# Optimization experiments

Hardware: AMD Instinct MI355X
Metric: run time of the kernel (lower is better)

The kernel has to match this reference:

```python
import jax, jax.numpy as jnp
import numpy as np

B, IN, OUT = 4, 32, 64
N, NS = 163842, 40962  # icosahedron mesh levels: NS = (N + 6) / 4
EPS = 1e-5
SLOPE = 0.2


def setup_inputs() -> dict:
    key = jax.random.key(0)
    ks = jax.random.split(key, 8)
    x = jax.random.normal(ks[0], (B, IN, N), dtype=jnp.float32)
    x1 = jax.random.normal(ks[1], (B, OUT, NS), dtype=jnp.float32)
    pool_neigh = jax.random.randint(ks[2], (NS * 7,), 0, N, dtype=jnp.int32)
    neigh = jax.random.randint(ks[3], (NS * 7,), 0, NS, dtype=jnp.int32)
    W1 = jax.random.normal(ks[4], (OUT, 7 * IN), dtype=jnp.float32) / np.sqrt(7 * IN).astype(np.float32)
    b1 = jnp.zeros((OUT,), dtype=jnp.float32)
    gamma = jnp.ones((OUT,), dtype=jnp.float32)
    beta = jnp.zeros((OUT,), dtype=jnp.float32)
    Wc = jax.random.normal(ks[5], (OUT, 2 * OUT), dtype=jnp.float32) / np.sqrt(2 * OUT).astype(np.float32)
    bc = jnp.zeros((OUT,), dtype=jnp.float32)
    return dict(x=x, x1=x1, pool_neigh=pool_neigh, neigh=neigh,
                W1=W1, b1=b1, gamma=gamma, beta=beta, Wc=Wc, bc=bc)


def reference(x, x1, pool_neigh, neigh, W1, b1, gamma, beta, Wc, bc):
    b, c, n = x.shape
    ns = (n + 6) // 4
    # pool_layer_batch ('mean'): gather 7-neighborhood on fine mesh, mean-pool
    pooled = x[:, :, pool_neigh[: ns * 7]].reshape(b, c, ns, 7).mean(axis=3)  # [B, IN, NS]
    # onering_conv_layer_batch: gather 7-stencil, reshape to [B, NS, 7*IN], linear
    mat = pooled[:, :, neigh].reshape(b, c, ns, 7)          # [B, IN, NS, 7]
    mat = mat.transpose(0, 2, 3, 1).reshape(b, ns, 7 * c)   # [B, NS, 7*IN]
    h = jnp.einsum('bnk,ok->bon', mat, W1) + b1[None, :, None]  # [B, OUT, NS]
    # BatchNorm1d (track_running_stats=False -> always batch stats) + LeakyReLU(0.2)
    mu = h.mean(axis=(0, 2), keepdims=True)
    var = h.var(axis=(0, 2), keepdims=True)
    h = gamma[None, :, None] * (h - mu) * jax.lax.rsqrt(var + EPS) + beta[None, :, None]
    h = jnp.where(h >= 0, h, SLOPE * h)
    # concat skip + 1x1 Conv1d
    cat = jnp.concatenate([h, x1], axis=1)                  # [B, 2*OUT, NS]
    out = jnp.einsum('bcn,oc->bon', cat, Wc) + bc[None, :, None]
    return out
```

## Files before the change

kernel.cpp:

```cpp
#include <hip/hip_runtime.h>
#include <cstddef>

#define NB    4
#define CIN   32
#define COUT  64
#define NFINE 163842
#define NSV   40962
#define EPSB  1e-5f
#define SLOPE 0.2f

typedef __attribute__((ext_vector_type(8))) short short8;
typedef __attribute__((ext_vector_type(4))) float f32x4;

#define O_XT   ((size_t)0)
#define O_H    ((size_t)0)
#define O_POOL ((size_t)48 << 20)
#define O_W1F  ((size_t)60 << 20)
#define O_WCF  ((size_t)60 << 20 | 0x8000)
#define O_ST   ((size_t)61 << 20)

static __device__ __forceinline__ short f2bf(float f) {
    union { float f; unsigned u; } v; v.f = f;
    unsigned r = v.u + 0x7fffu + ((v.u >> 16) & 1u);
    return (short)(r >> 16);
}
static __device__ __forceinline__ float bf2f(short h) {
    union { unsigned u; float f; } v;
    v.u = ((unsigned)(unsigned short)h) << 16;
    return v.f;
}

__global__ void k_prep(const float* __restrict__ W1, const float* __restrict__ Wc,
                       short* __restrict__ W1f, short* __restrict__ Wcf,
                       float* __restrict__ stats) {
    if (threadIdx.x < 128) stats[threadIdx.x] = 0.f;
    for (int i = threadIdx.x; i < 7 * 4 * 64 * 8; i += 256) {
        int e = i & 7, l = (i >> 3) & 63, nf = (i >> 9) & 3, kk = i >> 11;
        int o = 16 * nf + (l & 15);
        int k = 32 * kk + 8 * (l >> 4) + e;
        W1f[i] = f2bf(W1[o * (7 * CIN) + k]);
    }
    for (int i = threadIdx.x; i < 4 * 4 * 64 * 8; i += 256) {
        int e = i & 7, l = (i >> 3) & 63, nf = (i >> 9) & 3, kk = i >> 11;
        int o = 16 * nf + (l & 15);
        int c = 32 * kk + 8 * (l >> 4) + e;
        Wcf[i] = f2bf(Wc[o * (2 * COUT) + c]);
    }
}

__global__ __launch_bounds__(256) void k_transpose(
        const float* __restrict__ x, short* __restrict__ xt) {
    __shared__ float tile[128][33];
    const int n0 = blockIdx.x * 128;
    const int b  = blockIdx.y;
    const float* xb = x + (size_t)b * CIN * NFINE;
#pragma unroll
    for (int q = 0; q < 16; ++q) {
        int i = threadIdx.x + 256 * q;
        int c = i >> 7, nl = i & 127;
        int n = n0 + nl;
        tile[nl][c] = (n < NFINE) ? xb[(size_t)c * NFINE + n] : 0.f;
    }
    __syncthreads();
#pragma unroll
    for (int q = 0; q < 2; ++q) {
        int i = threadIdx.x + 256 * q;
        int nl = i >> 2, cg = i & 3;
        int n = n0 + nl;
        if (n >= NFINE) continue;
        short8 o;
#pragma unroll
        for (int e = 0; e < 8; ++e) o[e] = f2bf(tile[nl][8 * cg + e]);
        *(short8*)(xt + ((size_t)b * NFINE + n) * CIN + 8 * cg) = o;
    }
}

__global__ __launch_bounds__(256) void k_pool(
        const short* __restrict__ xt, const int* __restrict__ pn,
        short* __restrict__ pooled) {
    const int s = blockIdx.x * 256 + threadIdx.x;
    const int b = blockIdx.y;
    if (s >= NSV) return;
    int t[7];
#pragma unroll
    for (int j = 0; j < 7; ++j) t[j] = pn[7 * s + j];
    const short* xb = xt + (size_t)b * NFINE * CIN;
    short* op = pooled + ((size_t)b * NSV + s) * CIN;
#pragma unroll
    for (int gq = 0; gq < 4; ++gq) {
        short8 v[7];
#pragma unroll
        for (int j = 0; j < 7; ++j)
            v[j] = *(const short8*)(xb + (size_t)t[j] * CIN + 8 * gq);
        float a8[8];
#pragma unroll
        for (int e = 0; e < 8; ++e) a8[e] = 0.f;
#pragma unroll
        for (int j = 0; j < 7; ++j)
#pragma unroll
            for (int e = 0; e < 8; ++e) a8[e] += bf2f(v[j][e]);
        short8 o;
#pragma unroll
        for (int e = 0; e < 8; ++e) o[e] = f2bf(a8[e] * (1.f / 7.f));
        *(short8*)(op + 8 * gq) = o;
    }
}

__global__ __launch_bounds__(256) void k_conv(
        const int* __restrict__ neigh, const short* __restrict__ W1f,
        const short* __restrict__ pooled, short* __restrict__ hbf,
        float* __restrict__ stats) {
    __shared__ float red[2][4][COUT];
    const int l = threadIdx.x & 63, w = threadIdx.x >> 6;
    const int b = blockIdx.y;
    const int s0 = blockIdx.x * 128 + w * 32;
    const int r = l & 15, g = l >> 4;

    const short* pb = pooled + (size_t)b * NSV * CIN;
    const int sA0 = s0 + r, sA1 = s0 + 16 + r;
    const bool v0 = sA0 < NSV, v1 = sA1 < NSV;
    const int c0 = v0 ? sA0 : NSV - 1, c1 = v1 ? sA1 : NSV - 1;

    int t0[7], t1[7];
#pragma unroll
    for (int kk = 0; kk < 7; ++kk) { t0[kk] = neigh[7 * c0 + kk]; t1[kk] = neigh[7 * c1 + kk]; }

    short8 a0[7], a1[7];
#pragma unroll
    for (int kk = 0; kk < 7; ++kk) {
        a0[kk] = *(const short8*)(pb + (size_t)t0[kk] * CIN + 8 * g);
        a1[kk] = *(const short8*)(pb + (size_t)t1[kk] * CIN + 8 * g);
    }

    f32x4 acc[2][4];
#pragma unroll
    for (int mf = 0; mf < 2; ++mf)
#pragma unroll
        for (int nf = 0; nf < 4; ++nf) acc[mf][nf] = (f32x4){0.f, 0.f, 0.f, 0.f};

#pragma unroll
    for (int kk = 0; kk < 7; ++kk) {
        const short8* wf = (const short8*)(W1f) + (size_t)kk * 256;
#pragma unroll
        for (int nf = 0; nf < 4; ++nf) {
            short8 bfv = wf[nf * 64 + l];
            acc[0][nf] = __builtin_amdgcn_mfma_f32_16x16x32_bf16(a0[kk], bfv, acc[0][nf], 0, 0, 0);
            acc[1][nf] = __builtin_amdgcn_mfma_f32_16x16x32_bf16(a1[kk], bfv, acc[1][nf], 0, 0, 0);
        }
    }

    float sum[4], sq[4];
#pragma unroll
    for (int nf = 0; nf < 4; ++nf) { sum[nf] = 0.f; sq[nf] = 0.f; }
#pragma unroll
    for (int mf = 0; mf < 2; ++mf)
#pragma unroll
        for (int nf = 0; nf < 4; ++nf) {
            f32x4 d = acc[mf][nf];
#pragma unroll
            for (int rr = 0; rr < 4; ++rr) {
                const int srow = s0 + 16 * mf + 4 * g + rr;
                const float v = d[rr];
                const bool ok = srow < NSV;
                if (ok) hbf[((size_t)b * NSV + srow) * COUT + 16 * nf + r] = f2bf(v);
                const float vm = ok ? v : 0.f;
                sum[nf] += vm; sq[nf] += vm * vm;
            }
        }
#pragma unroll
    for (int nf = 0; nf < 4; ++nf) {
        float a = sum[nf], c = sq[nf];
        a += __shfl_xor(a, 16); a += __shfl_xor(a, 32);
        c += __shfl_xor(c, 16); c += __shfl_xor(c, 32);
        if (g == 0) { red[0][w][16 * nf + r] = a; red[1][w][16 * nf + r] = c; }
    }
    __syncthreads();
    if (threadIdx.x < COUT) {
        const int o = threadIdx.x;
        atomicAdd(&stats[o],        red[0][0][o] + red[0][1][o] + red[0][2][o] + red[0][3][o]);
        atomicAdd(&stats[COUT + o], red[1][0][o] + red[1][1][o] + red[1][2][o] + red[1][3][o]);
    }
}

__global__ void k_stats(const float* __restrict__ gamma,
                        const float* __restrict__ beta, float* __restrict__ st) {
    const int o = threadIdx.x;
    const float cnt = (float)((size_t)NB * NSV);
    float mu  = st[o] / cnt;
    float var = st[COUT + o] / cnt - mu * mu;
    float sc  = gamma[o] * rsqrtf(var + EPSB);
    st[2 * COUT + o] = sc;
    st[3 * COUT + o] = beta[o] - mu * sc;
}

__global__ __launch_bounds__(256) void k_out(
        const short* __restrict__ hbf, const float* __restrict__ x1,
        const short* __restrict__ Wcf, const float* __restrict__ st,
        const float* __restrict__ bc, float* __restrict__ out) {
    __shared__ __attribute__((aligned(16))) short Wcs[4 * 4 * 64 * 8];
    __shared__ float scs[COUT], shs[COUT], bcs[COUT];
    {
        const short8* src = (const short8*)Wcf;
        short8* dst = (short8*)Wcs;
        for (int i = threadIdx.x; i < 1024; i += 256) dst[i] = src[i];
        if (threadIdx.x < COUT) {
            scs[threadIdx.x] = st[2 * COUT + threadIdx.x];
            shs[threadIdx.x] = st[3 * COUT + threadIdx.x];
            bcs[threadIdx.x] = bc[threadIdx.x];
        }
    }
    __syncthreads();

    const int l = threadIdx.x & 63, w = threadIdx.x >> 6;
    const int b = blockIdx.y;
    const int s0 = blockIdx.x * 128 + w * 32;
    const int r = l & 15, g = l >> 4;

    int sa0 = s0 + r;       if (sa0 > NSV - 1) sa0 = NSV - 1;
    int sa1 = s0 + 16 + r;  if (sa1 > NSV - 1) sa1 = NSV - 1;
    const size_t rowA0 = ((size_t)b * NSV + sa0) * COUT;
    const size_t rowA1 = ((size_t)b * NSV + sa1) * COUT;

    short8 h00 = *(const short8*)(hbf + rowA0 + 8 * g);
    short8 h01 = *(const short8*)(hbf + rowA0 + 32 + 8 * g);
    short8 h10 = *(const short8*)(hbf + rowA1 + 8 * g);
    short8 h11 = *(const short8*)(hbf + rowA1 + 32 + 8 * g);
    const float* x1b = x1 + (size_t)b * COUT * NSV;
    float xv0[16], xv1[16];
#pragma unroll
    for (int i = 0; i < 16; ++i) {
        const int c2 = 32 * (i >> 3) + 8 * g + (i & 7);
        xv0[i] = x1b[(size_t)c2 * NSV + sa0];
        xv1[i] = x1b[(size_t)c2 * NSV + sa1];
    }

    float scv[16], shv[16];
#pragma unroll
    for (int kk = 0; kk < 2; ++kk)
#pragma unroll
        for (int e = 0; e < 8; ++e) {
            scv[8 * kk + e] = scs[32 * kk + 8 * g + e];
            shv[8 * kk + e] = shs[32 * kk + 8 * g + e];
        }

    f32x4 acc[2][4];
#pragma unroll
    for (int mf = 0; mf < 2; ++mf)
#pragma unroll
        for (int nf = 0; nf < 4; ++nf) acc[mf][nf] = (f32x4){0.f, 0.f, 0.f, 0.f};

#pragma unroll
    for (int kk = 0; kk < 4; ++kk) {
        short8 a0, a1;
        if (kk < 2) {
            short8 hh0 = kk ? h01 : h00;
            short8 hh1 = kk ? h11 : h10;
#pragma unroll
            for (int e = 0; e < 8; ++e) {
                float z0 = scv[8 * kk + e] * bf2f(hh0[e]) + shv[8 * kk + e];
                float z1 = scv[8 * kk + e] * bf2f(hh1[e]) + shv[8 * kk + e];
                z0 = fmaxf(z0, SLOPE * z0);
                z1 = fmaxf(z1, SLOPE * z1);
                a0[e] = f2bf(z0); a1[e] = f2bf(z1);
            }
        } else {
#pragma unroll
            for (int e = 0; e < 8; ++e) {
                a0[e] = f2bf(xv0[8 * (kk - 2) + e]);
                a1[e] = f2bf(xv1[8 * (kk - 2) + e]);
            }
        }
        const short8* wf = (const short8*)Wcs + kk * 4 * 64;
#pragma unroll
        for (int nf = 0; nf < 4; ++nf) {
            short8 bfv = wf[nf * 64 + l];
            acc[0][nf] = __builtin_amdgcn_mfma_f32_16x16x32_bf16(a0, bfv, acc[0][nf], 0, 0, 0);
            acc[1][nf] = __builtin_amdgcn_mfma_f32_16x16x32_bf16(a1, bfv, acc[1][nf], 0, 0, 0);
        }
    }

    float* ob = out + (size_t)b * COUT * NSV;
#pragma unroll
    for (int mf = 0; mf < 2; ++mf)
#pragma unroll
        for (int nf = 0; nf < 4; ++nf) {
            const int o  = 16 * nf + r;
            const int sr = s0 + 16 * mf + 4 * g;
            f32x4 d = acc[mf][nf];
            const float bb = bcs[o];
            float* p = ob + (size_t)o * NSV + sr;
            if (sr + 3 < NSV) {
                *(float2*)(p)     = make_float2(d[0] + bb, d[1] + bb);
                *(float2*)(p + 2) = make_float2(d[2] + bb, d[3] + bb);
            } else {
#pragma unroll
                for (int rr = 0; rr < 4; ++rr)
                    if (sr + rr < NSV) p[rr] = d[rr] + bb;
            }
        }
}

extern "C" void kernel_launch(void* const* d_in, const int* in_sizes, int n_in,
                              void* d_out, int out_size, void* d_ws, size_t ws_size,
                              hipStream_t stream) {
    const float* x          = (const float*)d_in[0];
    const float* x1         = (const float*)d_in[1];
    const int*   pool_neigh = (const int*)d_in[2];
    const int*   neigh      = (const int*)d_in[3];
    const float* W1         = (const float*)d_in[4];
    const float* gamma      = (const float*)d_in[6];
    const float* beta       = (const float*)d_in[7];
    const float* Wc         = (const float*)d_in[8];
    const float* bc         = (const float*)d_in[9];

    char* wsb = (char*)d_ws;
    short* xt     = (short*)(wsb + O_XT);
    short* hbf    = (short*)(wsb + O_H);
    short* pooled = (short*)(wsb + O_POOL);
    short* W1f    = (short*)(wsb + O_W1F);
    short* Wcf    = (short*)(wsb + O_WCF);
    float* stats  = (float*)(wsb + O_ST);
    float* out    = (float*)d_out;

    k_prep<<<1, 256, 0, stream>>>(W1, Wc, W1f, Wcf, stats);
    k_transpose<<<dim3((NFINE + 127) / 128, NB), 256, 0, stream>>>(x, xt);
    k_pool<<<dim3((NSV + 255) / 256, NB), 256, 0, stream>>>(xt, pool_neigh, pooled);
    k_conv<<<dim3((NSV + 127) / 128, NB), 256, 0, stream>>>(neigh, W1f, pooled, hbf, stats);
    k_stats<<<1, 64, 0, stream>>>(gamma, beta, stats);
    k_out<<<dim3((NSV + 127) / 128, NB), 256, 0, stream>>>(hbf, x1, Wcf, stats, bc, out);
}
```

Measured before the change: 342.9 us.

## Fold prep and stats kernels into neighbors; split pool work per channel group

Weight repacking and stats zeroing move into block (0,0) of the transpose kernel, and the BN scale/shift finalization moves into each k_out block's prologue. Together these remove two small kernel launches. The pool kernel now gives each thread one 8-channel group instead of all four, so there are four times as many threads and more gathers in flight. The cost is one transpose block doing extra serial work, every k_out block recomputing the stats, and each pool thread reloading its 7 neighbor indices.

```diff
diff --git a/kernel.cpp b/kernel.cpp
--- a/kernel.cpp
+++ b/kernel.cpp
@@ -30,26 +30,11 @@
     return v.f;
 }
 
-__global__ void k_prep(const float* __restrict__ W1, const float* __restrict__ Wc,
-                       short* __restrict__ W1f, short* __restrict__ Wcf,
-                       float* __restrict__ stats) {
-    if (threadIdx.x < 128) stats[threadIdx.x] = 0.f;
-    for (int i = threadIdx.x; i < 7 * 4 * 64 * 8; i += 256) {
-        int e = i & 7, l = (i >> 3) & 63, nf = (i >> 9) & 3, kk = i >> 11;
-        int o = 16 * nf + (l & 15);
-        int k = 32 * kk + 8 * (l >> 4) + e;
-        W1f[i] = f2bf(W1[o * (7 * CIN) + k]);
-    }
-    for (int i = threadIdx.x; i < 4 * 4 * 64 * 8; i += 256) {
-        int e = i & 7, l = (i >> 3) & 63, nf = (i >> 9) & 3, kk = i >> 11;
-        int o = 16 * nf + (l & 15);
-        int c = 32 * kk + 8 * (l >> 4) + e;
-        Wcf[i] = f2bf(Wc[o * (2 * COUT) + c]);
-    }
-}
-
 __global__ __launch_bounds__(256) void k_transpose(
-        const float* __restrict__ x, short* __restrict__ xt) {
+        const float* __restrict__ x, short* __restrict__ xt,
+        const float* __restrict__ W1, const float* __restrict__ Wc,
+        short* __restrict__ W1f, short* __restrict__ Wcf,
+        float* __restrict__ stats) {
     __shared__ float tile[128][33];
     const int n0 = blockIdx.x * 128;
     const int b  = blockIdx.y;
@@ -73,37 +58,49 @@
         for (int e = 0; e < 8; ++e) o[e] = f2bf(tile[nl][8 * cg + e]);
         *(short8*)(xt + ((size_t)b * NFINE + n) * CIN + 8 * cg) = o;
     }
+    if (blockIdx.x == 0 && blockIdx.y == 0) {
+        if (threadIdx.x < 128) stats[threadIdx.x] = 0.f;
+        for (int i = threadIdx.x; i < 7 * 4 * 64 * 8; i += 256) {
+            int e = i & 7, l = (i >> 3) & 63, nf = (i >> 9) & 3, kk = i >> 11;
+            int o = 16 * nf + (l & 15);
+            int k = 32 * kk + 8 * (l >> 4) + e;
+            W1f[i] = f2bf(W1[o * (7 * CIN) + k]);
+        }
+        for (int i = threadIdx.x; i < 4 * 4 * 64 * 8; i += 256) {
+            int e = i & 7, l = (i >> 3) & 63, nf = (i >> 9) & 3, kk = i >> 11;
+            int o = 16 * nf + (l & 15);
+            int c = 32 * kk + 8 * (l >> 4) + e;
+            Wcf[i] = f2bf(Wc[o * (2 * COUT) + c]);
+        }
+    }
 }
 
 __global__ __launch_bounds__(256) void k_pool(
         const short* __restrict__ xt, const int* __restrict__ pn,
         short* __restrict__ pooled) {
-    const int s = blockIdx.x * 256 + threadIdx.x;
+    const int gid = blockIdx.x * 256 + threadIdx.x;
+    const int s = gid >> 2, gq = gid & 3;
     const int b = blockIdx.y;
     if (s >= NSV) return;
     int t[7];
 #pragma unroll
     for (int j = 0; j < 7; ++j) t[j] = pn[7 * s + j];
-    const short* xb = xt + (size_t)b * NFINE * CIN;
-    short* op = pooled + ((size_t)b * NSV + s) * CIN;
-#pragma unroll
-    for (int gq = 0; gq < 4; ++gq) {
-        short8 v[7];
-#pragma unroll
-        for (int j = 0; j < 7; ++j)
-            v[j] = *(const short8*)(xb + (size_t)t[j] * CIN + 8 * gq);
-        float a8[8];
-#pragma unroll
-        for (int e = 0; e < 8; ++e) a8[e] = 0.f;
-#pragma unroll
-        for (int j = 0; j < 7; ++j)
-#pragma unroll
-            for (int e = 0; e < 8; ++e) a8[e] += bf2f(v[j][e]);
-        short8 o;
-#pragma unroll
-        for (int e = 0; e < 8; ++e) o[e] = f2bf(a8[e] * (1.f / 7.f));
-        *(short8*)(op + 8 * gq) = o;
-    }
+    const short* xb = xt + (size_t)b * NFINE * CIN + 8 * gq;
+    short8 v[7];
+#pragma unroll
+    for (int j = 0; j < 7; ++j)
+        v[j] = *(const short8*)(xb + (size_t)t[j] * CIN);
+    float a8[8];
+#pragma unroll
+    for (int e = 0; e < 8; ++e) a8[e] = 0.f;
+#pragma unroll
+    for (int j = 0; j < 7; ++j)
+#pragma unroll
+        for (int e = 0; e < 8; ++e) a8[e] += bf2f(v[j][e]);
+    short8 o;
+#pragma unroll
+    for (int e = 0; e < 8; ++e) o[e] = f2bf(a8[e] * (1.f / 7.f));
+    *(short8*)(pooled + ((size_t)b * NSV + s) * CIN + 8 * gq) = o;
 }
 
 __global__ __launch_bounds__(256) void k_conv(
@@ -182,20 +179,10 @@
     }
 }
 
-__global__ void k_stats(const float* __restrict__ gamma,
-                        const float* __restrict__ beta, float* __restrict__ st) {
-    const int o = threadIdx.x;
-    const float cnt = (float)((size_t)NB * NSV);
-    float mu  = st[o] / cnt;
-    float var = st[COUT + o] / cnt - mu * mu;
-    float sc  = gamma[o] * rsqrtf(var + EPSB);
-    st[2 * COUT + o] = sc;
-    st[3 * COUT + o] = beta[o] - mu * sc;
-}
-
 __global__ __launch_bounds__(256) void k_out(
         const short* __restrict__ hbf, const float* __restrict__ x1,
         const short* __restrict__ Wcf, const float* __restrict__ st,
+        const float* __restrict__ gamma, const float* __restrict__ beta,
         const float* __restrict__ bc, float* __restrict__ out) {
     __shared__ __attribute__((aligned(16))) short Wcs[4 * 4 * 64 * 8];
     __shared__ float scs[COUT], shs[COUT], bcs[COUT];
@@ -204,9 +191,14 @@
         short8* dst = (short8*)Wcs;
         for (int i = threadIdx.x; i < 1024; i += 256) dst[i] = src[i];
         if (threadIdx.x < COUT) {
-            scs[threadIdx.x] = st[2 * COUT + threadIdx.x];
-            shs[threadIdx.x] = st[3 * COUT + threadIdx.x];
-            bcs[threadIdx.x] = bc[threadIdx.x];
+            const int o = threadIdx.x;
+            const float cnt = (float)((size_t)NB * NSV);
+            float mu  = st[o] / cnt;
+            float var = st[COUT + o] / cnt - mu * mu;
+            float sc  = gamma[o] * rsqrtf(var + EPSB);
+            scs[o] = sc;
+            shs[o] = beta[o] - mu * sc;
+            bcs[o] = bc[o];
         }
     }
     __syncthreads();
@@ -322,10 +314,10 @@
     float* stats  = (float*)(wsb + O_ST);
     float* out    = (float*)d_out;
 
-    k_prep<<<1, 256, 0, stream>>>(W1, Wc, W1f, Wcf, stats);
-    k_transpose<<<dim3((NFINE + 127) / 128, NB), 256, 0, stream>>>(x, xt);
-    k_pool<<<dim3((NSV + 255) / 256, NB), 256, 0, stream>>>(xt, pool_neigh, pooled);
+    k_transpose<<<dim3((NFINE + 127) / 128, NB), 256, 0, stream>>>(
+        x, xt, W1, Wc, W1f, Wcf, stats);
+    k_pool<<<dim3((NSV * 4 + 255) / 256, NB), 256, 0, stream>>>(xt, pool_neigh, pooled);
     k_conv<<<dim3((NSV + 127) / 128, NB), 256, 0, stream>>>(neigh, W1f, pooled, hbf, stats);
-    k_stats<<<1, 64, 0, stream>>>(gamma, beta, stats);
-    k_out<<<dim3((NSV + 127) / 128, NB), 256, 0, stream>>>(hbf, x1, Wcf, stats, bc, out);
-}
+    k_out<<<dim3((NSV + 127) / 128, NB), 256, 0, stream>>>(
+        hbf, x1, Wcf, stats, gamma, beta, bc, out);
+}
```

New measurement: 276.6 us. 1.24x faster.
